# Kernel tuning notes

Measured on AMD Instinct MI355X. Metric: run time of the kernel, lower is better.

The kernel has to match this reference:

```python
import jax, jax.numpy as jnp
import numpy as np

B, S, R, D, A, P = 64, 128, 8, 10000, 10, 256


def setup_inputs() -> dict:
    key = jax.random.key(0)
    ks = jax.random.split(key, 7)
    return {
        "atom_hvs": jax.random.normal(ks[0], (A, D), jnp.float32),
        "pos_hvs": jax.random.normal(ks[1], (S, D), jnp.float32),
        "closure_tag": jax.random.normal(ks[2], (D,), jnp.float32),
        "W": jax.random.normal(ks[3], (P, D), jnp.float32) / np.float32(np.sqrt(D)),
        "b": jax.random.normal(ks[4], (P,), jnp.float32) * 0.01,
        "token_mask": jnp.ones((B, S), jnp.float32),
        "ring_mask": jnp.ones((B, R), jnp.float32),
        "atom_idx": jax.random.randint(ks[5], (B, S), 0, A),
        "ring_pos": jax.random.randint(ks[6], (B, R, 2), 0, S),
    }


def reference(atom_hvs, pos_hvs, closure_tag, W, b, token_mask, ring_mask, atom_idx, ring_pos):
    # HRR bind = circular convolution -> pointwise multiply in rFFT domain.
    # Bundle = sum; by linearity we sum in the frequency domain and do a
    # single irfft per molecule (same math as per-token conv + add).
    d = atom_hvs.shape[-1]
    Fa = jnp.fft.rfft(atom_hvs, axis=-1)          # [A, F]
    Fp = jnp.fft.rfft(pos_hvs, axis=-1)           # [S, F]
    Fc = jnp.fft.rfft(closure_tag)                # [F]

    s = atom_idx.shape[1]
    tok = Fa[atom_idx] * Fp[None, :s, :]          # [B, S, F] gather+bind
    freq = jnp.sum(token_mask[..., None] * tok, axis=1)   # [B, F] bundle

    ring = Fp[ring_pos[..., 0]] * Fp[ring_pos[..., 1]] * Fc  # [B, R, F]
    freq = freq + jnp.sum(ring_mask[..., None] * ring, axis=1)

    mol_hv = jnp.fft.irfft(freq, n=d, axis=-1)    # [B, D]
    return mol_hv @ W.T + b                       # [B, proj_dim]
```

## Files before the change

kernel.cpp:

```cpp
#include <hip/hip_runtime.h>

#define PI2 6.28318530717958647692f

#define NSIG 139
#define FS   5120

__global__ __launch_bounds__(256) void k_fwd(
                     const float* __restrict__ atom, const float* __restrict__ pos,
                     const float* __restrict__ clo, float2* __restrict__ spec) {
  __shared__ float xs[10000];
  unsigned sig = blockIdx.x, q = blockIdx.y;
  unsigned k1base = q * 10u;
  unsigned nk1 = (k1base + 10u <= 51u) ? 10u : (51u - k1base);
  const float* xb = (sig < 128u) ? (pos + sig * 10000u)
                   : ((sig < 138u) ? (atom + (sig - 128u) * 10000u) : clo);
  int tid = threadIdx.x;
  for (int i = tid; i < 2500; i += 256)
    *(float4*)(xs + 4 * i) = *(const float4*)(xb + 4 * i);
  __syncthreads();

  float resA[8], resB[8];
  unsigned ntile1 = nk1 * 25u;
  unsigned k1l = tid / 25u, n2 = (tid % 25u) * 4u;
  bool have = (unsigned)tid < ntile1;
  if (have) {
    unsigned k1 = k1base + k1l;
    float cth, sth;
    __sincosf(PI2 * (float)k1 * 0.01f, &sth, &cth);
    float c = 1.0f, s = 0.0f;
    float ar[4] = {}, as[4] = {};
#pragma unroll 4
    for (int n1 = 0; n1 < 100; ++n1) {
      const float4 xv = *(const float4*)(xs + n1 * 100 + n2);
      ar[0] += xv.x * c; as[0] += xv.x * s;
      ar[1] += xv.y * c; as[1] += xv.y * s;
      ar[2] += xv.z * c; as[2] += xv.z * s;
      ar[3] += xv.w * c; as[3] += xv.w * s;
      float cn = c * cth - s * sth;
      float sn = s * cth + c * sth;
      c = cn; s = sn;
    }
    unsigned rb = (100u - k1) % 100u;
#pragma unroll
    for (int j = 0; j < 4; ++j) {
      float swA, cwA, swB, cwB;
      __sincosf(PI2 * (float)((n2 + j) * k1) * 1e-4f, &swA, &cwA);
      __sincosf(PI2 * (float)((n2 + j) * rb) * 1e-4f, &swB, &cwB);
      resA[2 * j + 0] = ar[j] * cwA - as[j] * swA;
      resA[2 * j + 1] = -(as[j] * cwA + ar[j] * swA);
      resB[2 * j + 0] = ar[j] * cwB + as[j] * swB;
      resB[2 * j + 1] = as[j] * cwB - ar[j] * swB;
    }
  }
  __syncthreads();

  if (have) {
    float* pA = xs + k1l * 200u + n2 * 2u;
    float* pB = xs + (nk1 + k1l) * 200u + n2 * 2u;
    *(float4*)(pA + 0) = make_float4(resA[0], resA[1], resA[2], resA[3]);
    *(float4*)(pA + 4) = make_float4(resA[4], resA[5], resA[6], resA[7]);
    *(float4*)(pB + 0) = make_float4(resB[0], resB[1], resB[2], resB[3]);
    *(float4*)(pB + 4) = make_float4(resB[4], resB[5], resB[6], resB[7]);
  }
  __syncthreads();

  unsigned nrow = 2u * nk1;
  unsigned ntile3 = nrow * 26u;
  for (unsigned t = tid; t < ntile3; t += 256u) {
    unsigned lr = t / 26u, k2 = (t % 26u) * 2u;
    unsigned gk1 = (lr < nk1) ? (k1base + lr) : ((100u - (k1base + (lr - nk1))) % 100u);
    const float* brow = xs + lr * 200u;
    float cthA, sthA, cthB, sthB;
    __sincosf(PI2 * (float)k2 * 0.01f, &sthA, &cthA);
    __sincosf(PI2 * (float)(k2 + 1) * 0.01f, &sthB, &cthB);
    float cA = 1.0f, sA = 0.0f, cB = 1.0f, sB = 0.0f;
    float reA = 0.f, imA = 0.f, reB = 0.f, imB = 0.f;
#pragma unroll 4
    for (int n2i = 0; n2i < 100; n2i += 2) {
      const float4 b0 = *(const float4*)(brow + 2 * n2i);
      reA += b0.x * cA + b0.y * sA;  imA += b0.y * cA - b0.x * sA;
      reB += b0.x * cB + b0.y * sB;  imB += b0.y * cB - b0.x * sB;
      float cA1 = cA * cthA - sA * sthA, sA1 = sA * cthA + cA * sthA;
      float cB1 = cB * cthB - sB * sthB, sB1 = sB * cthB + cB * sthB;
      reA += b0.z * cA1 + b0.w * sA1;  imA += b0.w * cA1 - b0.z * sA1;
      reB += b0.z * cB1 + b0.w * sB1;  imB += b0.w * cB1 - b0.z * sB1;
      cA = cA1 * cthA - sA1 * sthA; sA = sA1 * cthA + cA1 * sthA;
      cB = cB1 * cthB - sB1 * sthB; sB = sB1 * cthB + cB1 * sthB;
    }
    unsigned kA = gk1 + 100u * k2;
    unsigned kB = gk1 + 100u * (k2 + 1);
    if (kA <= 5000u) spec[sig * FS + kA] = make_float2(reA, imA);
    if (kB <= 5000u) spec[sig * FS + kB] = make_float2(reB, imB);
  }
}

__global__ void k_mix(const float2* __restrict__ spec,
                      const float* __restrict__ tmask, const float* __restrict__ rmask,
                      const int* __restrict__ aidx, const int* __restrict__ rpos,
                      float2* __restrict__ G) {
  __shared__ float2 FaS[10][256];
  __shared__ float2 FcS[256];
  __shared__ float tmS[2][128];
  __shared__ int   aiS[2][128];
  __shared__ float rmS[2][8];
  __shared__ int   rpS[2][8][2];
  int tid = threadIdx.x;
  int k = blockIdx.x * 256 + tid;
  int kc = k > 5000 ? 5000 : k;
  int b0 = blockIdx.y * 2;
#pragma unroll
  for (int a = 0; a < 10; ++a) FaS[a][tid] = spec[(128 + a) * FS + kc];
  FcS[tid] = spec[138 * FS + kc];
  for (int i = tid; i < 2 * 128; i += 256) {
    int bb = i >> 7, ss = i & 127;
    tmS[bb][ss] = tmask[(b0 + bb) * 128 + ss];
    aiS[bb][ss] = aidx[(b0 + bb) * 128 + ss];
  }
  if (tid < 16) {
    int bb = tid >> 3, rr = tid & 7;
    rmS[bb][rr] = rmask[(b0 + bb) * 8 + rr];
    rpS[bb][rr][0] = rpos[((b0 + bb) * 8 + rr) * 2 + 0];
    rpS[bb][rr][1] = rpos[((b0 + bb) * 8 + rr) * 2 + 1];
  }
  __syncthreads();
  float fr[2] = {}, fi[2] = {};
#pragma unroll 8
  for (int s = 0; s < 128; ++s) {
    float2 fp = spec[s * FS + kc];
#pragma unroll
    for (int b = 0; b < 2; ++b) {
      int a = aiS[b][s];
      float tm = tmS[b][s];
      float2 fa = FaS[a][tid];
      float tr = fa.x * fp.x - fa.y * fp.y;
      float ti = fa.x * fp.y + fa.y * fp.x;
      fr[b] += tm * tr;
      fi[b] += tm * ti;
    }
  }
  float2 fc = FcS[tid];
#pragma unroll
  for (int r = 0; r < 8; ++r) {
#pragma unroll
    for (int b = 0; b < 2; ++b) {
      int p0 = rpS[b][r][0], p1 = rpS[b][r][1];
      float rm = rmS[b][r];
      float2 f0 = spec[p0 * FS + kc];
      float2 f1 = spec[p1 * FS + kc];
      float tr = f0.x * f1.x - f0.y * f1.y;
      float ti = f0.x * f1.y + f0.y * f1.x;
      float ur = tr * fc.x - ti * fc.y;
      float ui = tr * fc.y + ti * fc.x;
      fr[b] += rm * ur;
      fi[b] += rm * ui;
    }
  }
  if (k <= 5000) {
#pragma unroll
    for (int b = 0; b < 2; ++b) {
      float fib = (k == 0 || k == 5000) ? 0.0f : fi[b];
      G[(size_t)(b0 + b) * 10000 + k] = make_float2(fr[b], fib);
      if (k >= 1 && k <= 4999)
        G[(size_t)(b0 + b) * 10000 + (10000 - k)] = make_float2(fr[b], -fib);
    }
  }
}

__global__ void k_i1(const float2* __restrict__ G, float2* __restrict__ Bi) {
  __shared__ float gs[10400];
  unsigned sig = blockIdx.x;
  const float* gp = (const float*)(G + sig * 10000u);
  for (int i = threadIdx.x; i < 2600; i += 256) {
    int row = i / 26, c4 = i % 26;
    *(float4*)(gs + row * 104 + c4 * 4) = *(const float4*)(gp + row * 200 + c4 * 4);
  }
  __syncthreads();
  unsigned tt = blockIdx.y * 256u + threadIdx.x;
  if (tt >= 1300u) return;
  unsigned m1 = (tt / 26u) * 2u, n2 = (tt % 26u) * 2u;
  float cthA, sthA, cthB, sthB;
  __sincosf(PI2 * (float)m1 * 0.01f, &sthA, &cthA);
  __sincosf(PI2 * (float)(m1 + 1) * 0.01f, &sthB, &cthB);
  float cA = 1.0f, sA = 0.0f, cB = 1.0f, sB = 0.0f;
  float reA[2] = {}, imA[2] = {};
  float reB[2] = {}, imB[2] = {};
#pragma unroll 4
  for (int n1 = 0; n1 < 100; ++n1) {
    const float4 gv = *(const float4*)(gs + n1 * 104 + n2 * 2);
    reA[0] += gv.x * cA - gv.y * sA;  imA[0] += gv.y * cA + gv.x * sA;
    reB[0] += gv.z * cA - gv.w * sA;  imB[0] += gv.w * cA + gv.z * sA;
    reA[1] += gv.x * cB - gv.y * sB;  imA[1] += gv.y * cB + gv.x * sB;
    reB[1] += gv.z * cB - gv.w * sB;  imB[1] += gv.w * cB + gv.z * sB;
    float cA1 = cA * cthA - sA * sthA, sA1 = sA * cthA + cA * sthA;
    float cB1 = cB * cthB - sB * sthB, sB1 = sB * cthB + cB * sthB;
    cA = cA1; sA = sA1; cB = cB1; sB = sB1;
  }
  float w0 = (n2 == 0 || n2 == 50) ? 0.5f : 1.0f;
  float w1 = (n2 == 50) ? 0.0f : 1.0f;
#pragma unroll
  for (int i = 0; i < 2; ++i) {
    float sw0, cw0, sw1, cw1;
    __sincosf(PI2 * (float)(n2 * (m1 + i)) * 1e-4f, &sw0, &cw0);
    __sincosf(PI2 * (float)((n2 + 1) * (m1 + i)) * 1e-4f, &sw1, &cw1);
    float4 outv;
    outv.x = (reA[i] * cw0 - imA[i] * sw0) * w0;
    outv.y = (imA[i] * cw0 + reA[i] * sw0) * w0;
    outv.z = (reB[i] * cw1 - imB[i] * sw1) * w1;
    outv.w = (imB[i] * cw1 + reB[i] * sw1) * w1;
    *(float4*)((float*)Bi + (sig * 5200u + (m1 + i) * 52u + n2) * 2) = outv;
  }
}

__global__ void k_i2(const float2* __restrict__ Bi, float* __restrict__ mol) {
  __shared__ float bs[10400];
  unsigned sig = blockIdx.x;
  const float* bp = (const float*)Bi + sig * 10400u;
  for (int i = threadIdx.x; i < 2600; i += 256)
    *(float4*)(bs + 4 * i) = *(const float4*)(bp + 4 * i);
  __syncthreads();
  unsigned tt = blockIdx.y * 256u + threadIdx.x;
  if (tt >= 2500u) return;
  unsigned m1 = (tt / 50u) * 2u;
  unsigned m2 = (tt % 50u) * 2u;
  const float* b0 = bs + m1 * 104u;
  const float* b1 = b0 + 104;
  float cthA, sthA, cthB, sthB;
  __sincosf(PI2 * (float)m2 * 0.01f, &sthA, &cthA);
  __sincosf(PI2 * (float)(m2 + 1) * 0.01f, &sthB, &cthB);
  float cA = 1.0f, sA = 0.0f, cB = 1.0f, sB = 0.0f;
  float re[2][2] = {};
#pragma unroll 4
  for (int jj = 0; jj < 26; ++jj) {
    int n2 = 2 * jj;
    const float4 v0 = *(const float4*)(b0 + 2 * n2);
    const float4 v1 = *(const float4*)(b1 + 2 * n2);
    re[0][0] += v0.x * cA - v0.y * sA;
    re[1][0] += v1.x * cA - v1.y * sA;
    re[0][1] += v0.x * cB - v0.y * sB;
    re[1][1] += v1.x * cB - v1.y * sB;
    float cA1 = cA * cthA - sA * sthA, sA1 = sA * cthA + cA * sthA;
    float cB1 = cB * cthB - sB * sthB, sB1 = sB * cthB + cB * sthB;
    re[0][0] += v0.z * cA1 - v0.w * sA1;
    re[1][0] += v1.z * cA1 - v1.w * sA1;
    re[0][1] += v0.z * cB1 - v0.w * sB1;
    re[1][1] += v1.z * cB1 - v1.w * sB1;
    cA = cA1 * cthA - sA1 * sthA; sA = sA1 * cthA + cA1 * sthA;
    cB = cB1 * cthB - sB1 * sthB; sB = sB1 * cthB + cB1 * sthB;
  }
#pragma unroll
  for (int i = 0; i < 2; ++i)
#pragma unroll
    for (int j = 0; j < 2; ++j)
      mol[sig * 10000u + (m1 + i) + 100u * (m2 + j)] = re[i][j] * 2e-4f;
}

__global__ __launch_bounds__(256) void k_proj(const float* __restrict__ mol,
                                              const float* __restrict__ W,
                                              float* __restrict__ part) {
  __shared__ float molS[40 * 64];
  int tid = threadIdx.x;
  int d0 = blockIdx.x * 40;
  for (int i = tid; i < 40 * 64; i += 256)
    molS[i] = mol[(size_t)(i & 63) * 10000 + d0 + (i >> 6)];
  __syncthreads();
  int p0 = (tid & 63) * 4;
  int bh = (tid >> 6) * 16;
  float acc[4][16] = {};
  const float* w0 = W + (size_t)(p0 + 0) * 10000 + d0;
  const float* w1 = W + (size_t)(p0 + 1) * 10000 + d0;
  const float* w2 = W + (size_t)(p0 + 2) * 10000 + d0;
  const float* w3 = W + (size_t)(p0 + 3) * 10000 + d0;
#pragma unroll 4
  for (int dl = 0; dl < 40; ++dl) {
    const float wv[4] = {w0[dl], w1[dl], w2[dl], w3[dl]};
    const float4* m4 = (const float4*)(molS + dl * 64 + bh);
#pragma unroll
    for (int q = 0; q < 4; ++q) {
      float4 mv = m4[q];
#pragma unroll
      for (int pp = 0; pp < 4; ++pp) {
        acc[pp][4 * q + 0] += wv[pp] * mv.x;
        acc[pp][4 * q + 1] += wv[pp] * mv.y;
        acc[pp][4 * q + 2] += wv[pp] * mv.z;
        acc[pp][4 * q + 3] += wv[pp] * mv.w;
      }
    }
  }
#pragma unroll
  for (int b = 0; b < 16; ++b) {
    float4 v = make_float4(acc[0][b], acc[1][b], acc[2][b], acc[3][b]);
    *(float4*)(part + (size_t)blockIdx.x * 16384 + (bh + b) * 256 + p0) = v;
  }
}

__global__ void k_red(const float* __restrict__ part, const float* __restrict__ bias,
                      float* __restrict__ out) {
  int tid = threadIdx.x;
  int b = blockIdx.x;
  float acc = bias[tid];
#pragma unroll 8
  for (int ch = 0; ch < 250; ++ch)
    acc += part[(size_t)ch * 16384 + b * 256 + tid];
  out[b * 256 + tid] = acc;
}

extern "C" void kernel_launch(void* const* d_in, const int* in_sizes, int n_in,
                              void* d_out, int out_size, void* d_ws, size_t ws_size,
                              hipStream_t stream) {
  const float* atom  = (const float*)d_in[0];
  const float* pos   = (const float*)d_in[1];
  const float* clo   = (const float*)d_in[2];
  const float* W     = (const float*)d_in[3];
  const float* bias  = (const float*)d_in[4];
  const float* tmask = (const float*)d_in[5];
  const float* rmask = (const float*)d_in[6];
  const int*   aidx  = (const int*)d_in[7];
  const int*   rpos  = (const int*)d_in[8];
  float* out = (float*)d_out;

  char* ws = (char*)d_ws;
  size_t off = 0;
  auto alloc = [&](size_t n) { off = (off + 255) & ~(size_t)255; size_t o = off; off += n; return o; };
  char* regA   = ws + alloc(16777216);
  float2* Bi   = (float2*)regA;
  float*  part = (float*)regA;
  float2* spec = (float2*)(ws + alloc((size_t)NSIG * FS * 8));
  float2* G    = (float2*)(ws + alloc((size_t)64 * 10000 * 8));
  float*  mol  = (float*)(ws + alloc((size_t)64 * 10000 * 4));

  k_fwd<<<dim3(NSIG, 6), dim3(256), 0, stream>>>(atom, pos, clo, spec);
  k_mix<<<dim3(20, 32), dim3(256), 0, stream>>>(spec, tmask, rmask, aidx, rpos, G);
  k_i1<<<dim3(64, 6), dim3(256), 0, stream>>>(G, Bi);
  k_i2<<<dim3(64, 10), dim3(256), 0, stream>>>(Bi, mol);
  k_proj<<<dim3(250), dim3(256), 0, stream>>>(mol, W, part);
  k_red<<<dim3(64), dim3(256), 0, stream>>>(part, bias, out);
}
```

Before: 193.9 us.

## Transpose W and molecule vectors so projection loads coalesce

Adds a kernel that transposes W into a [D, P] layout on every call. k_i2 now writes the molecule vectors as [D, B], so the projection kernel can read both operands with coalesced, contiguous loads instead of strided per-row accesses. The projection grid is split over two batch halves and each thread now keeps 32 accumulators for a single output column. The cost is an extra full read and write of W (about 10 MB) per call, plus scattered stores from k_i2.

```diff
diff --git a/kernel.cpp b/kernel.cpp
--- a/kernel.cpp
+++ b/kernel.cpp
@@ -4,6 +4,24 @@
 
 #define NSIG 139
 #define FS   5120
+
+__global__ __launch_bounds__(256) void k_wt(const float* __restrict__ W,
+                                            float* __restrict__ Wt) {
+  __shared__ float t[64][65];
+  int d0 = blockIdx.x * 64, p0 = blockIdx.y * 64;
+  int lane = threadIdx.x % 64;
+  int row  = threadIdx.x / 64;
+  for (int r = row; r < 64; r += 4) {
+    int d = d0 + lane;
+    t[r][lane] = (d < 10000) ? W[(size_t)(p0 + r) * 10000 + d] : 0.0f;
+  }
+  __syncthreads();
+  for (int r = row; r < 64; r += 4) {
+    int d = d0 + r;
+    if (d < 10000)
+      Wt[(size_t)d * 256 + p0 + lane] = t[lane][r];
+  }
+}
 
 __global__ __launch_bounds__(256) void k_fwd(
                      const float* __restrict__ atom, const float* __restrict__ pos,
@@ -211,7 +229,7 @@
   }
 }
 
-__global__ void k_i2(const float2* __restrict__ Bi, float* __restrict__ mol) {
+__global__ void k_i2(const float2* __restrict__ Bi, float* __restrict__ molT) {
   __shared__ float bs[10400];
   unsigned sig = blockIdx.x;
   const float* bp = (const float*)Bi + sig * 10400u;
@@ -251,46 +269,39 @@
   for (int i = 0; i < 2; ++i)
 #pragma unroll
     for (int j = 0; j < 2; ++j)
-      mol[sig * 10000u + (m1 + i) + 100u * (m2 + j)] = re[i][j] * 2e-4f;
-}
-
-__global__ __launch_bounds__(256) void k_proj(const float* __restrict__ mol,
-                                              const float* __restrict__ W,
+      molT[(size_t)((m1 + i) + 100u * (m2 + j)) * 64u + sig] = re[i][j] * 2e-4f;
+}
+
+__global__ __launch_bounds__(256) void k_proj(const float* __restrict__ molT,
+                                              const float* __restrict__ Wt,
                                               float* __restrict__ part) {
-  __shared__ float molS[40 * 64];
+  __shared__ float molS[40 * 32];
   int tid = threadIdx.x;
   int d0 = blockIdx.x * 40;
-  for (int i = tid; i < 40 * 64; i += 256)
-    molS[i] = mol[(size_t)(i & 63) * 10000 + d0 + (i >> 6)];
-  __syncthreads();
-  int p0 = (tid & 63) * 4;
-  int bh = (tid >> 6) * 16;
-  float acc[4][16] = {};
-  const float* w0 = W + (size_t)(p0 + 0) * 10000 + d0;
-  const float* w1 = W + (size_t)(p0 + 1) * 10000 + d0;
-  const float* w2 = W + (size_t)(p0 + 2) * 10000 + d0;
-  const float* w3 = W + (size_t)(p0 + 3) * 10000 + d0;
+  int bh = blockIdx.y * 32;
+  for (int i = tid; i < 320; i += 256) {
+    int dl = (i * 4) / 32, bl = (i * 4) % 32;
+    *(float4*)(molS + dl * 32 + bl) = *(const float4*)(molT + (size_t)(d0 + dl) * 64 + bh + bl);
+  }
+  __syncthreads();
+  float acc[32] = {};
+  const float* wp = Wt + (size_t)d0 * 256 + tid;
 #pragma unroll 4
   for (int dl = 0; dl < 40; ++dl) {
-    const float wv[4] = {w0[dl], w1[dl], w2[dl], w3[dl]};
-    const float4* m4 = (const float4*)(molS + dl * 64 + bh);
-#pragma unroll
-    for (int q = 0; q < 4; ++q) {
+    float w = wp[dl * 256];
+    const float4* m4 = (const float4*)(molS + dl * 32);
+#pragma unroll
+    for (int q = 0; q < 8; ++q) {
       float4 mv = m4[q];
-#pragma unroll
-      for (int pp = 0; pp < 4; ++pp) {
-        acc[pp][4 * q + 0] += wv[pp] * mv.x;
-        acc[pp][4 * q + 1] += wv[pp] * mv.y;
-        acc[pp][4 * q + 2] += wv[pp] * mv.z;
-        acc[pp][4 * q + 3] += wv[pp] * mv.w;
-      }
-    }
-  }
-#pragma unroll
-  for (int b = 0; b < 16; ++b) {
-    float4 v = make_float4(acc[0][b], acc[1][b], acc[2][b], acc[3][b]);
-    *(float4*)(part + (size_t)blockIdx.x * 16384 + (bh + b) * 256 + p0) = v;
-  }
+      acc[4 * q + 0] += w * mv.x;
+      acc[4 * q + 1] += w * mv.y;
+      acc[4 * q + 2] += w * mv.z;
+      acc[4 * q + 3] += w * mv.w;
+    }
+  }
+#pragma unroll
+  for (int b = 0; b < 32; ++b)
+    part[(size_t)blockIdx.x * 16384 + (bh + b) * 256 + tid] = acc[b];
 }
 
 __global__ void k_red(const float* __restrict__ part, const float* __restrict__ bias,
@@ -326,12 +337,14 @@
   float*  part = (float*)regA;
   float2* spec = (float2*)(ws + alloc((size_t)NSIG * FS * 8));
   float2* G    = (float2*)(ws + alloc((size_t)64 * 10000 * 8));
-  float*  mol  = (float*)(ws + alloc((size_t)64 * 10000 * 4));
-
+  float*  molT = (float*)(ws + alloc((size_t)10000 * 64 * 4));
+  float*  Wt   = (float*)(ws + alloc((size_t)10000 * 256 * 4));
+
+  k_wt<<<dim3(157, 4), dim3(256), 0, stream>>>(W, Wt);
   k_fwd<<<dim3(NSIG, 6), dim3(256), 0, stream>>>(atom, pos, clo, spec);
   k_mix<<<dim3(20, 32), dim3(256), 0, stream>>>(spec, tmask, rmask, aidx, rpos, G);
   k_i1<<<dim3(64, 6), dim3(256), 0, stream>>>(G, Bi);
-  k_i2<<<dim3(64, 10), dim3(256), 0, stream>>>(Bi, mol);
-  k_proj<<<dim3(250), dim3(256), 0, stream>>>(mol, W, part);
+  k_i2<<<dim3(64, 10), dim3(256), 0, stream>>>(Bi, molT);
+  k_proj<<<dim3(250, 2), dim3(256), 0, stream>>>(molT, Wt, part);
   k_red<<<dim3(64), dim3(256), 0, stream>>>(part, bias, out);
 }
```

Result: slower. 199.8 us (+3.1%).
